# Performance work log

Measured on AMD Instinct MI355X. Metric: run time of the kernel, lower is better.

## Reference

```python
import jax, jax.numpy as jnp
import numpy as np

N_AGENTS, BATCH, SDIM, ADIM = 8, 16384, 64, 16
HID, HEADS = 128, 4
ATT_D = HID // HEADS  # 32
EPS = 1e-5


def _bn(x):
    # BatchNorm1d(affine=False), training-mode stats over batch axis (axis=1), biased var
    m = x.mean(axis=1, keepdims=True)
    v = ((x - m) ** 2).mean(axis=1, keepdims=True)
    return (x - m) * jax.lax.rsqrt(v + EPS)


def setup_inputs() -> dict:
    key = jax.random.key(0)
    ks = jax.random.split(key, 16)
    sc = lambda *sh: 1.0 / np.sqrt(sh[-2] if len(sh) > 1 else sh[-1])
    inp = {
        "s": jax.random.normal(ks[0], (N_AGENTS, BATCH, SDIM), jnp.float32),
        "a": jax.random.uniform(ks[1], (N_AGENTS, BATCH, ADIM), jnp.float32),
        # per-agent sa encoder (Attention_Actor): Linear(sdim+adim, hid)
        "W_sa": jax.random.normal(ks[2], (N_AGENTS, SDIM + ADIM, HID), jnp.float32) * (1.0 / np.sqrt(SDIM + ADIM)),
        "b_sa": jnp.zeros((N_AGENTS, HID), jnp.float32),
        # per-agent state encoder: Linear(sdim, hid)
        "W_se": jax.random.normal(ks[3], (N_AGENTS, SDIM, HID), jnp.float32) * (1.0 / np.sqrt(SDIM)),
        "b_se": jnp.zeros((N_AGENTS, HID), jnp.float32),
        # per-head key/selector (no bias) and value (with bias) extractors, shared across agents
        "Wk": jax.random.normal(ks[4], (HEADS, HID, ATT_D), jnp.float32) * (1.0 / np.sqrt(HID)),
        "Wsel": jax.random.normal(ks[5], (HEADS, HID, ATT_D), jnp.float32) * (1.0 / np.sqrt(HID)),
        "Wv": jax.random.normal(ks[6], (HEADS, HID, ATT_D), jnp.float32) * (1.0 / np.sqrt(HID)),
        "bv": jnp.zeros((HEADS, ATT_D), jnp.float32),
        # per-agent critic: Linear(2*hid, hid) -> LeakyReLU -> Linear(hid, adim)
        "Wc1": jax.random.normal(ks[7], (N_AGENTS, 2 * HID, HID), jnp.float32) * (1.0 / np.sqrt(2 * HID)),
        "bc1": jnp.zeros((N_AGENTS, HID), jnp.float32),
        "Wc2": jax.random.normal(ks[8], (N_AGENTS, HID, ADIM), jnp.float32) * (1.0 / np.sqrt(HID)),
        "bc2": jnp.zeros((N_AGENTS, ADIM), jnp.float32),
    }
    return inp


def reference(s, a, W_sa, b_sa, W_se, b_se, Wk, Wsel, Wv, bv, Wc1, bc1, Wc2, bc2):
    lrelu = jax.nn.leaky_relu  # slope 0.01 like nn.LeakyReLU default
    # sa encodings: BN -> Linear -> LeakyReLU, per agent  [N,B,H]
    sa = _bn(jnp.concatenate([s, a], axis=-1))
    e = lrelu(jnp.einsum('nbi,nih->nbh', sa, W_sa) + b_sa[:, None, :])
    # state encodings  [N,B,H]
    se = lrelu(jnp.einsum('nbi,nih->nbh', _bn(s), W_se) + b_se[:, None, :])
    # per-head projections  [P,N,B,D]
    keys = jnp.einsum('nbh,phd->pnbd', e, Wk)
    vals = lrelu(jnp.einsum('nbh,phd->pnbd', e, Wv) + bv[:, None, None, :])
    sel = jnp.einsum('nbh,phd->pnbd', se, Wsel)
    # attention of agent i over agents j != i  [P,N,N,B]
    logits = jnp.einsum('pibd,pjbd->pijb', sel, keys) / np.sqrt(ATT_D).astype(np.float32)
    self_mask = jnp.eye(N_AGENTS, dtype=bool)[None, :, :, None]
    w = jax.nn.softmax(jnp.where(self_mask, -1e9, logits), axis=2)
    other = jnp.einsum('pijb,pjbd->pibd', w, vals)  # [P,N,B,D]
    other_flat = jnp.transpose(other, (1, 2, 0, 3)).reshape(N_AGENTS, BATCH, HEADS * ATT_D)
    # critic: concat(s_enc, head values) -> MLP -> gather Q at argmax action
    critic_in = jnp.concatenate([se, other_flat], axis=-1)  # [N,B,2H]
    h = lrelu(jnp.einsum('nbi,nih->nbh', critic_in, Wc1) + bc1[:, None, :])
    all_q = jnp.einsum('nbh,nho->nbo', h, Wc2) + bc2[:, None, :]  # [N,B,adim]
    int_acs = jnp.argmax(a, axis=-1)[..., None]  # [N,B,1]
    q = jnp.take_along_axis(all_q, int_acs, axis=-1)  # [N,B,1]
    return q
```

## Files before the change

kernel.cpp:

```cpp
#include <hip/hip_runtime.h>


typedef unsigned short u16;
typedef unsigned int u32;

#define NA 8
#define BATCH 16384
#define SD 64
#define AD 16
#define IND 80
#define HID 128
#define HEADS 4
#define ATT 32
#define EPS 1e-5f
#define KP 136
#define KP3 104
#define KPS 72
#define VTS 68
#define WBS 24

using short8 = __attribute__((ext_vector_type(8))) short;
using float4f = __attribute__((ext_vector_type(4))) float;
#define MFMA16(a, b, c) __builtin_amdgcn_mfma_f32_16x16x32_bf16((a), (b), (c), 0, 0, 0)

__device__ __forceinline__ float bf2f(u16 u) { union { u32 i; float f; } v; v.i = ((u32)u) << 16; return v.f; }
__device__ __forceinline__ float lo2f(u32 w) { union { u32 i; float f; } v; v.i = w << 16; return v.f; }
__device__ __forceinline__ float hi2f(u32 w) { union { u32 i; float f; } v; v.i = w & 0xffff0000u; return v.f; }
__device__ __forceinline__ u16 f2bf(float f) {
  union { float f; u32 i; } v; v.f = f;
  u32 x = v.i;
  x += 0x7fffu + ((x >> 16) & 1u);
  return (u16)(x >> 16);
}
__device__ __forceinline__ float lrelu(float x) { return x > 0.f ? x : 0.01f * x; }
__device__ __forceinline__ float ldin(const void* p, size_t i, bool bf) {
  return bf ? bf2f(((const u16*)p)[i]) : ((const float*)p)[i];
}
__device__ __forceinline__ u16 ldbf(const void* p, size_t i, bool bf) {
  return bf ? ((const u16*)p)[i] : f2bf(((const float*)p)[i]);
}
__device__ __forceinline__ short8 lds_s8(const u16* p) {
  union { short8 v; u32 u[4]; } t;
  const u32* q = (const u32*)p;
  t.u[0] = q[0]; t.u[1] = q[1]; t.u[2] = q[2]; t.u[3] = q[3];
  return t.v;
}
__device__ __forceinline__ void barlg() {
  asm volatile("s_waitcnt lgkmcnt(0)" ::: "memory");
  __builtin_amdgcn_s_barrier();
}

__global__ __launch_bounds__(256) void k_prep2(
    const void* __restrict__ s, const void* __restrict__ a,
    const void* __restrict__ Wsa, const void* __restrict__ Wse,
    const void* __restrict__ Wsl, const void* __restrict__ Wk, const void* __restrict__ Wv,
    const void* __restrict__ Wc1,
    int* __restrict__ flag, float* __restrict__ part,
    u16* __restrict__ Wsa_t, u16* __restrict__ Wse_t, u16* __restrict__ Wp_t, u16* __restrict__ Wc1t) {
  __shared__ u16 T[80 * 130];
  __shared__ float S0[256], Q0[256], S1[256], Q1[256];
  __shared__ int cnt[2];
  int tid = threadIdx.x;
  if (tid < 2) cnt[tid] = 0;
  __syncthreads();
  {
    u32 wv = ((const u32*)s)[tid];
    u32 lo = wv & 0xffffu, e = (lo >> 7) & 0xffu;
    if (lo == 0u || lo == 0x8000u) atomicAdd(&cnt[1], 1);
    else if (e < 0x70u || e > 0x8fu) atomicAdd(&cnt[0], 1);
  }
  __syncthreads();
  bool bf = !(cnt[0] >= 64 || cnt[1] >= 192);
  if (blockIdx.x == 0 && tid == 0) *flag = bf ? 1 : 0;
  int blkr = blockIdx.x;
  if (blkr < 2048) {
    int n = blkr >> 8, c = blkr & 255, b0 = c << 6;
    float* p = part + (size_t)(n * 256 + c) * 160;
    {
      int f2 = tid & 31, rg = tid >> 5;
      float s0 = 0.f, s1 = 0.f, q0 = 0.f, q1 = 0.f;
      #pragma unroll
      for (int i = 0; i < 8; i++) {
        int b = b0 + rg + 8 * i;
        float x0, x1;
        if (bf) { u32 wv = ((const u32*)s)[((size_t)n * BATCH + b) * 32 + f2]; x0 = lo2f(wv); x1 = hi2f(wv); }
        else { const float* sf = (const float*)s + ((size_t)n * BATCH + b) * 64 + 2 * f2; x0 = sf[0]; x1 = sf[1]; }
        s0 += x0; q0 += x0 * x0; s1 += x1; q1 += x1 * x1;
      }
      S0[tid] = s0; Q0[tid] = q0; S1[tid] = s1; Q1[tid] = q1;
    }
    __syncthreads();
    if (tid < 64) {
      int f2 = tid >> 1, odd = tid & 1;
      float S = 0.f, Q = 0.f;
      #pragma unroll
      for (int rg = 0; rg < 8; rg++) {
        int ix = rg * 32 + f2;
        S += odd ? S1[ix] : S0[ix];
        Q += odd ? Q1[ix] : Q0[ix];
      }
      p[tid * 2] = S; p[tid * 2 + 1] = Q;
    }
    __syncthreads();
    {
      int f2 = tid & 7, rg = tid >> 3;
      float s0 = 0.f, s1 = 0.f, q0 = 0.f, q1 = 0.f;
      #pragma unroll
      for (int i = 0; i < 2; i++) {
        int b = b0 + rg + 32 * i;
        float x0, x1;
        if (bf) { u32 wv = ((const u32*)a)[((size_t)n * BATCH + b) * 8 + f2]; x0 = lo2f(wv); x1 = hi2f(wv); }
        else { const float* af = (const float*)a + ((size_t)n * BATCH + b) * 16 + 2 * f2; x0 = af[0]; x1 = af[1]; }
        s0 += x0; q0 += x0 * x0; s1 += x1; q1 += x1 * x1;
      }
      S0[tid] = s0; Q0[tid] = q0; S1[tid] = s1; Q1[tid] = q1;
    }
    __syncthreads();
    if (tid < 16) {
      int f2 = tid >> 1, odd = tid & 1;
      float S = 0.f, Q = 0.f;
      #pragma unroll
      for (int rg = 0; rg < 32; rg++) {
        int ix = rg * 8 + f2;
        S += odd ? S1[ix] : S0[ix];
        Q += odd ? Q1[ix] : Q0[ix];
      }
      p[(SD + tid) * 2] = S; p[(SD + tid) * 2 + 1] = Q;
    }
    return;
  }
  int blk = blkr - 2048;
  if (blk < 32) {
    int n = blk >> 2, k0 = (blk & 3) * 64;
    for (int i = tid; i < 64 * 128; i += 256) {
      int kr = i >> 7, cc = i & 127;
      T[kr * 130 + cc] = ldbf(Wc1, ((size_t)n * 256 + k0 + kr) * 128 + cc, bf);
    }
    __syncthreads();
    for (int i = tid; i < 128 * 64; i += 256) {
      int col = i >> 6, kk = i & 63;
      Wc1t[((size_t)n * 128 + col) * 256 + k0 + kk] = T[kk * 130 + col];
    }
  } else if (blk < 40) {
    int n = blk - 32;
    for (int i = tid; i < 80 * 128; i += 256) {
      int kr = i >> 7, cc = i & 127;
      T[kr * 130 + cc] = ldbf(Wsa, ((size_t)n * IND + kr) * 128 + cc, bf);
    }
    __syncthreads();
    for (int i = tid; i < 128 * KP3; i += 256) {
      int col = i / KP3, k = i - col * KP3;
      Wsa_t[((size_t)n * 128 + col) * KP3 + k] = (k < IND) ? T[k * 130 + col] : (u16)0;
    }
  } else if (blk < 48) {
    int n = blk - 40;
    for (int i = tid; i < 64 * 128; i += 256) {
      int kr = i >> 7, cc = i & 127;
      T[kr * 130 + cc] = ldbf(Wse, ((size_t)n * SD + kr) * 128 + cc, bf);
    }
    __syncthreads();
    for (int i = tid; i < 128 * KPS; i += 256) {
      int col = i / KPS, k = i - col * KPS;
      Wse_t[((size_t)n * 128 + col) * KPS + k] = (k < SD) ? T[k * 130 + col] : (u16)0;
    }
  } else {
    int pm = blk - 48, p = pm / 3, mat = pm - 3 * p;
    const void* W = (mat == 0) ? Wsl : (mat == 1) ? Wk : Wv;
    for (int i = tid; i < 128 * 32; i += 256) {
      int kr = i >> 5, d = i & 31;
      T[kr * 34 + d] = ldbf(W, ((size_t)p * HID + kr) * ATT + d, bf);
    }
    __syncthreads();
    for (int i = tid; i < 32 * KP; i += 256) {
      int d = i / KP, k = i - d * KP;
      Wp_t[((size_t)mat * HID + p * ATT + d) * KP + k] = (k < HID) ? T[k * 34 + d] : (u16)0;
    }
  }
}

__global__ __launch_bounds__(256) void k_fin(const float* __restrict__ part, float* __restrict__ mst_g) {
  int n = blockIdx.x;
  int t = threadIdx.x;
  if (t < 160) {
    const float* p = part + (size_t)n * 256 * 160 + t;
    float acc = 0.f;
    #pragma unroll 8
    for (int c = 0; c < 256; c++) acc += p[(size_t)c * 160];
    float other = __shfl_xor(acc, 1);
    if ((t & 1) == 0) {
      float mean = acc * (1.f / BATCH);
      float var = other * (1.f / BATCH) - mean * mean;
      mst_g[(size_t)n * 160 + t] = mean;
      mst_g[(size_t)n * 160 + t + 1] = rsqrtf(var + EPS);
    }
  }
}

__global__ __launch_bounds__(256) void k_enc7(
    const void* __restrict__ s, const void* __restrict__ a,
    const u16* __restrict__ Wsa_t, const void* __restrict__ bsa,
    const u16* __restrict__ Wse_t, const void* __restrict__ bse,
    const u16* __restrict__ Wp_t, const void* __restrict__ bv_g,
    const float* __restrict__ mst_g, const int* __restrict__ flag,
    u16* __restrict__ SEo, u16* __restrict__ SEL2, u16* __restrict__ KEY2, u16* __restrict__ VAL2) {
  __shared__ __align__(16) u16 A[64 * KP];
  __shared__ __align__(16) u16 Bt[64 * KP];
  __shared__ float mst[IND * 2];
  __shared__ float bsaf[HID], bsef[HID], bvf[HID];
  bool bf = (*flag != 0);
  int tid = threadIdx.x;
  int n = blockIdx.y;
  int b0 = blockIdx.x * 64;
  int w = tid >> 6, lane = tid & 63, q = lane >> 4, rl = lane & 15;
  if (tid < HID) {
    bsaf[tid] = ldin(bsa, n * HID + tid, bf);
    bsef[tid] = ldin(bse, n * HID + tid, bf);
    bvf[tid]  = ldin(bv_g, tid, bf);
  }
  if (tid < IND * 2) mst[tid] = mst_g[(size_t)n * IND * 2 + tid];
  barlg();
  for (int i = tid; i < 64 * 32; i += 256) {
    int row = i >> 5, kp = i & 31;
    float x0, x1;
    if (bf) { u32 wv = ((const u32*)s)[((size_t)n * BATCH + b0 + row) * 32 + kp]; x0 = lo2f(wv); x1 = hi2f(wv); }
    else { const float* sf = (const float*)s + ((size_t)n * BATCH + b0 + row) * 64 + 2 * kp; x0 = sf[0]; x1 = sf[1]; }
    int k = 2 * kp;
    u32 o = (u32)f2bf((x0 - mst[k * 2]) * mst[k * 2 + 1]) |
            ((u32)f2bf((x1 - mst[k * 2 + 2]) * mst[k * 2 + 3]) << 16);
    *(u32*)&A[row * KP + k] = o;
  }
  for (int i = tid; i < 64 * 8; i += 256) {
    int row = i >> 3, kp = i & 7;
    float x0, x1;
    if (bf) { u32 wv = ((const u32*)a)[((size_t)n * BATCH + b0 + row) * 8 + kp]; x0 = lo2f(wv); x1 = hi2f(wv); }
    else { const float* af = (const float*)a + ((size_t)n * BATCH + b0 + row) * 16 + 2 * kp; x0 = af[0]; x1 = af[1]; }
    int k = SD + 2 * kp;
    u32 o = (u32)f2bf((x0 - mst[k * 2]) * mst[k * 2 + 1]) |
            ((u32)f2bf((x1 - mst[k * 2 + 2]) * mst[k * 2 + 3]) << 16);
    *(u32*)&A[row * KP + k] = o;
  }
  for (int i = tid; i < 64 * 8; i += 256) {
    int row = i >> 3, c2 = i & 7;
    *(u32*)&A[row * KP + IND + 2 * c2] = 0u;
  }
  barlg();
  const u16* WS = Wse_t + (size_t)n * HID * KPS;
  const u16* WA = Wsa_t + (size_t)n * HID * KP3;
  {
    float4f accS[8] = {};
    #pragma unroll
    for (int kc = 0; kc < 2; kc++) {
      short8 a0 = *(const short8*)&A[(w * 16 + rl) * KP + kc * 32 + q * 8];
      #pragma unroll
      for (int nt = 0; nt < 8; nt++) {
        short8 bb = *(const short8*)(WS + (size_t)(nt * 16 + rl) * KPS + kc * 32 + q * 8);
        accS[nt] = MFMA16(a0, bb, accS[nt]);
      }
    }
    #pragma unroll
    for (int nt = 0; nt < 8; nt++)
      #pragma unroll
      for (int r = 0; r < 4; r++) {
        int row = w * 16 + q * 4 + r, col = nt * 16 + rl;
        u16 v = f2bf(lrelu(accS[nt][r] + bsef[col]));
        SEo[((size_t)n * BATCH + b0 + row) * HID + col] = v;
        Bt[row * KP + col] = v;
      }
  }
  __builtin_amdgcn_sched_barrier(0);
  {
    float4f accE[8] = {};
    #pragma unroll
    for (int kc = 0; kc < 3; kc++) {
      short8 a0 = *(const short8*)&A[(w * 16 + rl) * KP + kc * 32 + q * 8];
      #pragma unroll
      for (int nt = 0; nt < 8; nt++) {
        short8 bb = *(const short8*)(WA + (size_t)(nt * 16 + rl) * KP3 + kc * 32 + q * 8);
        accE[nt] = MFMA16(a0, bb, accE[nt]);
      }
    }
    barlg();
    #pragma unroll
    for (int nt = 0; nt < 8; nt++)
      #pragma unroll
      for (int r = 0; r < 4; r++) {
        int row = w * 16 + q * 4 + r, col = nt * 16 + rl;
        A[row * KP + col] = f2bf(lrelu(accE[nt][r] + bsaf[col]));
      }
  }
  barlg();
  const u16* WSL = Wp_t;
  const u16* WKm = Wp_t + (size_t)HID * KP;
  const u16* WVm = Wp_t + (size_t)2 * HID * KP;
  {
    float4f ac[4][2] = {};
    #pragma unroll
    for (int kc = 0; kc < 4; kc++) {
      short8 af[4];
      #pragma unroll
      for (int mt = 0; mt < 4; mt++)
        af[mt] = *(const short8*)&A[(mt * 16 + rl) * KP + kc * 32 + q * 8];
      #pragma unroll
      for (int nt = 0; nt < 2; nt++) {
        short8 bk = *(const short8*)(WKm + (size_t)(w * 32 + nt * 16 + rl) * KP + kc * 32 + q * 8);
        #pragma unroll
        for (int mt = 0; mt < 4; mt++)
          ac[mt][nt] = MFMA16(af[mt], bk, ac[mt][nt]);
      }
    }
    #pragma unroll
    for (int mt = 0; mt < 4; mt++)
      #pragma unroll
      for (int nt = 0; nt < 2; nt++)
        #pragma unroll
        for (int r = 0; r < 4; r++) {
          int row = mt * 16 + q * 4 + r, col = w * 32 + nt * 16 + rl;
          KEY2[((size_t)(b0 + row) * NA + n) * HID + col] = f2bf(ac[mt][nt][r]);
        }
  }
  __builtin_amdgcn_sched_barrier(0);
  {
    float4f ac[4][2] = {};
    #pragma unroll
    for (int kc = 0; kc < 4; kc++) {
      short8 af[4];
      #pragma unroll
      for (int mt = 0; mt < 4; mt++)
        af[mt] = *(const short8*)&A[(mt * 16 + rl) * KP + kc * 32 + q * 8];
      #pragma unroll
      for (int nt = 0; nt < 2; nt++) {
        short8 bv8 = *(const short8*)(WVm + (size_t)(w * 32 + nt * 16 + rl) * KP + kc * 32 + q * 8);
        #pragma unroll
        for (int mt = 0; mt < 4; mt++)
          ac[mt][nt] = MFMA16(af[mt], bv8, ac[mt][nt]);
      }
    }
    #pragma unroll
    for (int mt = 0; mt < 4; mt++)
      #pragma unroll
      for (int nt = 0; nt < 2; nt++)
        #pragma unroll
        for (int r = 0; r < 4; r++) {
          int row = mt * 16 + q * 4 + r, col = w * 32 + nt * 16 + rl;
          VAL2[((size_t)(b0 + row) * NA + n) * HID + col] = f2bf(lrelu(ac[mt][nt][r] + bvf[col]));
        }
  }
  __builtin_amdgcn_sched_barrier(0);
  {
    float4f ac[4][2] = {};
    #pragma unroll
    for (int kc = 0; kc < 4; kc++) {
      short8 af[4];
      #pragma unroll
      for (int mt = 0; mt < 4; mt++)
        af[mt] = *(const short8*)&Bt[(mt * 16 + rl) * KP + kc * 32 + q * 8];
      #pragma unroll
      for (int nt = 0; nt < 2; nt++) {
        short8 bl = *(const short8*)(WSL + (size_t)(w * 32 + nt * 16 + rl) * KP + kc * 32 + q * 8);
        #pragma unroll
        for (int mt = 0; mt < 4; mt++)
          ac[mt][nt] = MFMA16(af[mt], bl, ac[mt][nt]);
      }
    }
    #pragma unroll
    for (int mt = 0; mt < 4; mt++)
      #pragma unroll
      for (int nt = 0; nt < 2; nt++)
        #pragma unroll
        for (int r = 0; r < 4; r++) {
          int row = mt * 16 + q * 4 + r, col = w * 32 + nt * 16 + rl;
          SEL2[((size_t)(b0 + row) * NA + n) * HID + col] = f2bf(ac[mt][nt][r]);
        }
  }
}

__global__ __launch_bounds__(256) void k_attn2(
    u16* SELO, const u16* __restrict__ KEY, const u16* __restrict__ VAL) {
  __shared__ __align__(16) u16 valt[HEADS * ATT * VTS];
  __shared__ u16 wb[64 * WBS];
  int tid = threadIdx.x;
  size_t r0 = (size_t)blockIdx.x * 64;
  int w = tid >> 6, lane = tid & 63, q = lane >> 4, rl = lane & 15;
  {
    const u32* vu = (const u32*)VAL;
    #pragma unroll
    for (int t = 0; t < 16; t++) {
      int idx = tid + t * 256;
      int rp = idx >> 6, c2 = idx & 63;
      u32 wv = vu[(r0 + rp) * 64 + c2];
      int c = 2 * c2;
      valt[c * VTS + rp] = (u16)(wv & 0xffffu);
      valt[(c + 1) * VTS + rp] = (u16)(wv >> 16);
    }
  }
  barlg();
  const float scale = 0.17677669529663687f;
  const size_t fbase = (r0 + w * 16 + rl) * HID;
  #pragma unroll
  for (int p = 0; p < HEADS; p++) {
    short8 sa = *(const short8*)(SELO + fbase + p * ATT + q * 8);
    short8 kb = *(const short8*)(KEY + fbase + p * ATT + q * 8);
    float4f zc = {};
    float4f c = MFMA16(sa, kb, zc);
    int nn = rl;
    #pragma unroll
    for (int r = 0; r < 4; r++) {
      int row = q * 4 + r;
      float x = c[r] * scale;
      if (row == nn) x = -1e9f;
      float mx = x;
      mx = fmaxf(mx, __shfl_xor(mx, 1));
      mx = fmaxf(mx, __shfl_xor(mx, 2));
      mx = fmaxf(mx, __shfl_xor(mx, 4));
      float e = __expf(x - mx);
      float ssum = e;
      ssum += __shfl_xor(ssum, 1);
      ssum += __shfl_xor(ssum, 2);
      ssum += __shfl_xor(ssum, 4);
      float wv = e / ssum;
      if ((row >> 3) != (nn >> 3)) wv = 0.f;
      wb[(w * 16 + row) * WBS + nn] = f2bf(wv);
    }
    short8 aw;
    if (q < 2) aw = *(const short8*)&wb[(w * 16 + rl) * WBS + q * 8];
    else { short8 z = {}; aw = z; }
    float4f o[2] = {};
    #pragma unroll
    for (int nt = 0; nt < 2; nt++) {
      short8 bv8 = lds_s8(&valt[(p * ATT + nt * 16 + rl) * VTS + w * 16 + (q & 1) * 8]);
      o[nt] = MFMA16(aw, bv8, o[nt]);
    }
    #pragma unroll
    for (int nt = 0; nt < 2; nt++)
      #pragma unroll
      for (int r = 0; r < 4; r++) {
        int row = q * 4 + r;
        int rp = w * 16 + (row >> 3) * 8 + (row & 7);
        SELO[(r0 + rp) * HID + p * ATT + nt * 16 + rl] = f2bf(o[nt][r]);
      }
  }
}

__global__ __launch_bounds__(256) void k_critic(
    const u16* __restrict__ SEi, const u16* __restrict__ OT, const void* __restrict__ a_g,
    const u16* __restrict__ Wc1t, const void* __restrict__ bc1_g,
    const void* __restrict__ Wc2_g, const void* __restrict__ bc2_g,
    const int* __restrict__ flag, void* __restrict__ qo) {
  __shared__ __align__(16) u16 Xt[128 * KP];
  __shared__ float wc2f[HID * AD];
  __shared__ float bc1f[HID];
  __shared__ int amax[128];
  bool bf = (*flag != 0);
  int tid = threadIdx.x;
  int n = blockIdx.y;
  int b0 = blockIdx.x * 128;
  int w = tid >> 6, lane = tid & 63, q = lane >> 4, rl = lane & 15;
  if (tid < HID) bc1f[tid] = ldin(bc1_g, n * HID + tid, bf);
  const u16* WT = Wc1t + (size_t)n * HID * 256;

  float4f acc[2][8] = {};
  for (int ph = 0; ph < 2; ph++) {
    for (int idx = tid; idx < 128 * 64; idx += 256) {
      int row = idx >> 6, c = idx & 63;
      u32 wv;
      if (ph == 0) wv = ((const u32*)SEi)[((size_t)n * BATCH + b0 + row) * 64 + c];
      else         wv = ((const u32*)OT)[((size_t)(b0 + row) * NA + n) * 64 + c];
      ((u32*)&Xt[row * KP])[c] = wv;
    }
    barlg();
    #pragma unroll
    for (int kc = 0; kc < 4; kc++) {
      int ko = ph * HID + kc * 32;
      short8 a0 = *(const short8*)&Xt[((2 * w) * 16 + rl) * KP + kc * 32 + q * 8];
      short8 a1 = *(const short8*)&Xt[((2 * w + 1) * 16 + rl) * KP + kc * 32 + q * 8];
      #pragma unroll
      for (int nt = 0; nt < 8; nt++) {
        short8 bb = *(const short8*)(WT + (size_t)(nt * 16 + rl) * 256 + ko + q * 8);
        acc[0][nt] = MFMA16(a0, bb, acc[0][nt]);
        acc[1][nt] = MFMA16(a1, bb, acc[1][nt]);
      }
    }
    barlg();
  }
  u16* ht = Xt;
  #pragma unroll
  for (int mi = 0; mi < 2; mi++)
    #pragma unroll
    for (int nt = 0; nt < 8; nt++)
      #pragma unroll
      for (int r = 0; r < 4; r++) {
        int row = (2 * w + mi) * 16 + q * 4 + r, col = nt * 16 + rl;
        ht[row * KP + col] = f2bf(lrelu(acc[mi][nt][r] + bc1f[col]));
      }
  for (int idx = tid; idx < HID * AD; idx += 256)
    wc2f[idx] = ldin(Wc2_g, (size_t)n * HID * AD + idx, bf);
  if (tid < 128) {
    size_t base = ((size_t)n * BATCH + b0 + tid) * AD;
    float best = ldin(a_g, base, bf); int bi = 0;
    for (int o = 1; o < AD; o++) {
      float v = ldin(a_g, base + o, bf);
      if (v > best) { best = v; bi = o; }
    }
    amax[tid] = bi;
  }
  barlg();
  {
    int b = tid >> 1, half = tid & 1;
    int col = amax[b];
    float acq = 0.f;
    const u16* hr = &ht[b * KP + half * 64];
    #pragma unroll
    for (int k = 0; k < 64; k++)
      acq = fmaf(bf2f(hr[k]), wc2f[(half * 64 + k) * AD + col], acq);
    acq += __shfl_xor(acq, 1);
    if (half == 0) {
      float v = acq + ldin(bc2_g, n * AD + col, bf);
      size_t oidx = (size_t)n * BATCH + b0 + b;
      if (bf) ((u16*)qo)[oidx] = f2bf(v);
      else    ((float*)qo)[oidx] = v;
    }
  }
}

extern "C" void kernel_launch(void* const* d_in, const int* in_sizes, int n_in,
                              void* d_out, int out_size, void* d_ws, size_t ws_size,
                              hipStream_t stream) {
  const void* s   = d_in[0];
  const void* a   = d_in[1];
  const void* Wsa = d_in[2];
  const void* bsa = d_in[3];
  const void* Wse = d_in[4];
  const void* bse = d_in[5];
  const void* Wk  = d_in[6];
  const void* Wsl = d_in[7];
  const void* Wv  = d_in[8];
  const void* bv  = d_in[9];
  const void* Wc1 = d_in[10];
  const void* bc1 = d_in[11];
  const void* Wc2 = d_in[12];
  const void* bc2 = d_in[13];

  char* ws = (char*)d_ws;
  int*   flag  = (int*)ws;
  float* part  = (float*)(ws + 1024);
  float* mst_g = (float*)(ws + 1311744);
  u16*   Wsa_t = (u16*)(ws + 1316864);
  u16*   Wse_t = (u16*)(ws + 1529856);
  u16*   Wp_t  = (u16*)(ws + 1677312);
  u16*   Wc1t  = (u16*)(ws + 1781760);
  u16*   SEb   = (u16*)(ws + 2306048);
  u16*   SEL   = (u16*)(ws + 2306048 + 1ull * 33554432ull);
  u16*   KEY   = (u16*)(ws + 2306048 + 2ull * 33554432ull);
  u16*   VAL   = (u16*)(ws + 2306048 + 3ull * 33554432ull);

  k_prep2<<<2108, 256, 0, stream>>>(s, a, Wsa, Wse, Wsl, Wk, Wv, Wc1,
                                    flag, part, Wsa_t, Wse_t, Wp_t, Wc1t);
  k_fin<<<NA, 256, 0, stream>>>(part, mst_g);
  k_enc7<<<dim3(BATCH / 64, NA), 256, 0, stream>>>(s, a, Wsa_t, bsa, Wse_t, bse, Wp_t, bv,
                                                   mst_g, flag, SEb, SEL, KEY, VAL);
  k_attn2<<<BATCH / 8, 256, 0, stream>>>(SEL, KEY, VAL);
  k_critic<<<dim3(BATCH / 128, NA), 256, 0, stream>>>(SEb, SEL, a, Wc1t, bc1, Wc2, bc2, flag, d_out);
}
```

Measured before the change: 262.6 us.

## Prefetch attention operands, retile critic GEMM per-wave columns, vectorize argmax

In the attention kernel, the first head's selector and key fragments are loaded before the value transpose and the barrier, and each later head's fragments are prefetched one iteration ahead, so global latency overlaps compute. The critic kernel now gives each wave 32 output columns across all 128 rows instead of 32 rows across all columns. Each wave therefore keeps only two weight fragments from global memory per k-chunk and reads the activation tiles from LDS. The argmax over actions uses vector loads split across two lanes, and it runs together with the Wc2 load before the GEMM; the final dot product reads LDS in short8 vectors. The cost is more LDS reads in the critic GEMM and slightly higher register pressure.

```diff
diff --git a/kernel.cpp b/kernel.cpp
--- a/kernel.cpp
+++ b/kernel.cpp
@@ -21,6 +21,7 @@
 
 using short8 = __attribute__((ext_vector_type(8))) short;
 using float4f = __attribute__((ext_vector_type(4))) float;
+using uint4v = __attribute__((ext_vector_type(4))) u32;
 #define MFMA16(a, b, c) __builtin_amdgcn_mfma_f32_16x16x32_bf16((a), (b), (c), 0, 0, 0)
 
 __device__ __forceinline__ float bf2f(u16 u) { union { u32 i; float f; } v; v.i = ((u32)u) << 16; return v.f; }
@@ -381,6 +382,9 @@
   int tid = threadIdx.x;
   size_t r0 = (size_t)blockIdx.x * 64;
   int w = tid >> 6, lane = tid & 63, q = lane >> 4, rl = lane & 15;
+  const size_t fbase = (r0 + w * 16 + rl) * HID;
+  short8 sa = *(const short8*)(SELO + fbase + q * 8);
+  short8 kb = *(const short8*)(KEY + fbase + q * 8);
   {
     const u32* vu = (const u32*)VAL;
     #pragma unroll
@@ -395,11 +399,13 @@
   }
   barlg();
   const float scale = 0.17677669529663687f;
-  const size_t fbase = (r0 + w * 16 + rl) * HID;
   #pragma unroll
   for (int p = 0; p < HEADS; p++) {
-    short8 sa = *(const short8*)(SELO + fbase + p * ATT + q * 8);
-    short8 kb = *(const short8*)(KEY + fbase + p * ATT + q * 8);
+    short8 nsa = sa, nkb = kb;
+    if (p < HEADS - 1) {
+      nsa = *(const short8*)(SELO + fbase + (p + 1) * ATT + q * 8);
+      nkb = *(const short8*)(KEY + fbase + (p + 1) * ATT + q * 8);
+    }
     float4f zc = {};
     float4f c = MFMA16(sa, kb, zc);
     int nn = rl;
@@ -438,10 +444,11 @@
         int rp = w * 16 + (row >> 3) * 8 + (row & 7);
         SELO[(r0 + rp) * HID + p * ATT + nt * 16 + rl] = f2bf(o[nt][r]);
       }
-  }
-}
-
-__global__ __launch_bounds__(256) void k_critic(
+    sa = nsa; kb = nkb;
+  }
+}
+
+__global__ __launch_bounds__(256) void k_critic2(
     const u16* __restrict__ SEi, const u16* __restrict__ OT, const void* __restrict__ a_g,
     const u16* __restrict__ Wc1t, const void* __restrict__ bc1_g,
     const void* __restrict__ Wc2_g, const void* __restrict__ bc2_g,
@@ -456,9 +463,34 @@
   int b0 = blockIdx.x * 128;
   int w = tid >> 6, lane = tid & 63, q = lane >> 4, rl = lane & 15;
   if (tid < HID) bc1f[tid] = ldin(bc1_g, n * HID + tid, bf);
+  {
+    int b = tid >> 1, half = tid & 1;
+    float best; int bi;
+    if (bf) {
+      const uint4v* pa = (const uint4v*)((const u32*)a_g + ((size_t)n * BATCH + b0 + b) * 8 + half * 4);
+      uint4v x = *pa;
+      float v[8] = {lo2f(x[0]), hi2f(x[0]), lo2f(x[1]), hi2f(x[1]),
+                    lo2f(x[2]), hi2f(x[2]), lo2f(x[3]), hi2f(x[3])};
+      best = v[0]; bi = 0;
+      #pragma unroll
+      for (int j = 1; j < 8; j++) if (v[j] > best) { best = v[j]; bi = j; }
+    } else {
+      const float* pa = (const float*)a_g + ((size_t)n * BATCH + b0 + b) * 16 + half * 8;
+      float4f v0 = *(const float4f*)pa, v1 = *(const float4f*)(pa + 4);
+      float v[8] = {v0[0], v0[1], v0[2], v0[3], v1[0], v1[1], v1[2], v1[3]};
+      best = v[0]; bi = 0;
+      #pragma unroll
+      for (int j = 1; j < 8; j++) if (v[j] > best) { best = v[j]; bi = j; }
+    }
+    float ob = __shfl_xor(best, 1);
+    int obi = __shfl_xor(bi, 1);
+    if (half == 0) amax[b] = (ob > best) ? (obi + 8) : bi;
+  }
+  for (int idx = tid; idx < HID * AD; idx += 256)
+    wc2f[idx] = ldin(Wc2_g, (size_t)n * HID * AD + idx, bf);
   const u16* WT = Wc1t + (size_t)n * HID * 256;
 
-  float4f acc[2][8] = {};
+  float4f acc[8][2] = {};
   for (int ph = 0; ph < 2; ph++) {
     for (int idx = tid; idx < 128 * 64; idx += 256) {
       int row = idx >> 6, c = idx & 63;
@@ -471,47 +503,41 @@
     #pragma unroll
     for (int kc = 0; kc < 4; kc++) {
       int ko = ph * HID + kc * 32;
-      short8 a0 = *(const short8*)&Xt[((2 * w) * 16 + rl) * KP + kc * 32 + q * 8];
-      short8 a1 = *(const short8*)&Xt[((2 * w + 1) * 16 + rl) * KP + kc * 32 + q * 8];
-      #pragma unroll
-      for (int nt = 0; nt < 8; nt++) {
-        short8 bb = *(const short8*)(WT + (size_t)(nt * 16 + rl) * 256 + ko + q * 8);
-        acc[0][nt] = MFMA16(a0, bb, acc[0][nt]);
-        acc[1][nt] = MFMA16(a1, bb, acc[1][nt]);
+      short8 bb0 = *(const short8*)(WT + (size_t)(w * 32 + rl) * 256 + ko + q * 8);
+      short8 bb1 = *(const short8*)(WT + (size_t)(w * 32 + 16 + rl) * 256 + ko + q * 8);
+      #pragma unroll
+      for (int mt = 0; mt < 8; mt++) {
+        short8 af = *(const short8*)&Xt[(mt * 16 + rl) * KP + kc * 32 + q * 8];
+        acc[mt][0] = MFMA16(af, bb0, acc[mt][0]);
+        acc[mt][1] = MFMA16(af, bb1, acc[mt][1]);
       }
     }
     barlg();
   }
   u16* ht = Xt;
   #pragma unroll
-  for (int mi = 0; mi < 2; mi++)
-    #pragma unroll
-    for (int nt = 0; nt < 8; nt++)
+  for (int mt = 0; mt < 8; mt++)
+    #pragma unroll
+    for (int nt = 0; nt < 2; nt++)
       #pragma unroll
       for (int r = 0; r < 4; r++) {
-        int row = (2 * w + mi) * 16 + q * 4 + r, col = nt * 16 + rl;
-        ht[row * KP + col] = f2bf(lrelu(acc[mi][nt][r] + bc1f[col]));
-      }
-  for (int idx = tid; idx < HID * AD; idx += 256)
-    wc2f[idx] = ldin(Wc2_g, (size_t)n * HID * AD + idx, bf);
-  if (tid < 128) {
-    size_t base = ((size_t)n * BATCH + b0 + tid) * AD;
-    float best = ldin(a_g, base, bf); int bi = 0;
-    for (int o = 1; o < AD; o++) {
-      float v = ldin(a_g, base + o, bf);
-      if (v > best) { best = v; bi = o; }
-    }
-    amax[tid] = bi;
-  }
+        int row = mt * 16 + q * 4 + r, col = w * 32 + nt * 16 + rl;
+        ht[row * KP + col] = f2bf(lrelu(acc[mt][nt][r] + bc1f[col]));
+      }
   barlg();
   {
     int b = tid >> 1, half = tid & 1;
     int col = amax[b];
     float acq = 0.f;
     const u16* hr = &ht[b * KP + half * 64];
-    #pragma unroll
-    for (int k = 0; k < 64; k++)
-      acq = fmaf(bf2f(hr[k]), wc2f[(half * 64 + k) * AD + col], acq);
+    const float* wz = &wc2f[(half * 64) * AD + col];
+    #pragma unroll
+    for (int kk = 0; kk < 8; kk++) {
+      short8 hv = lds_s8(hr + kk * 8);
+      #pragma unroll
+      for (int j = 0; j < 8; j++)
+        acq = fmaf(bf2f((u16)hv[j]), wz[(kk * 8 + j) * AD], acq);
+    }
     acq += __shfl_xor(acq, 1);
     if (half == 0) {
       float v = acq + ldin(bc2_g, n * AD + col, bf);
@@ -559,5 +585,5 @@
   k_enc7<<<dim3(BATCH / 64, NA), 256, 0, stream>>>(s, a, Wsa_t, bsa, Wse_t, bse, Wp_t, bv,
                                                    mst_g, flag, SEb, SEL, KEY, VAL);
   k_attn2<<<BATCH / 8, 256, 0, stream>>>(SEL, KEY, VAL);
-  k_critic<<<dim3(BATCH / 128, NA), 256, 0, stream>>>(SEb, SEL, a, Wc1t, bc1, Wc2, bc2, flag, d_out);
-}
+  k_critic2<<<dim3(BATCH / 128, NA), 256, 0, stream>>>(SEb, SEL, a, Wc1t, bc1, Wc2, bc2, flag, d_out);
+}
```

New measurement: 247.8 us. 5.7% less time.
